# Performance work log

Measured on AMD Instinct MI355X. Metric: run time of the kernel, lower is better.

## Reference

```python
import jax, jax.numpy as jnp
import numpy as np

B, C, K, D = 2048, 100, 8, 64


def setup_inputs() -> dict:
    key = jax.random.key(0)
    k1, k2, k3, k4 = jax.random.split(key, 4)
    representation = jax.random.normal(k1, (B, D), dtype=jnp.float32)
    mixture_logits = 0.1 * jax.random.normal(k2, (C, K), dtype=jnp.float32)
    loc = jax.random.normal(k3, (C, K, D), dtype=jnp.float32)
    # lower-triangular with unit diagonal, small off-diagonal (matches 'random'/'zeros' init style)
    raw = 0.05 * jax.random.normal(k4, (C, K, D, D), dtype=jnp.float32)
    scale_tril = jnp.tril(raw, k=-1) + jnp.eye(D, dtype=jnp.float32)
    return {"representation": representation, "mixture_logits": mixture_logits,
            "loc": loc, "scale_tril": scale_tril}


def reference(representation, mixture_logits, loc, scale_tril):
    # representation: [B, D]; mixture_logits: [C, K]; loc: [C, K, D]; scale_tril: [C, K, D, D]
    d = representation.shape[-1]
    log2pi = jnp.log(jnp.asarray(2.0 * np.pi, dtype=representation.dtype))
    # residuals: [B, C, K, D] -> move batch last for batched triangular solve: [C, K, D, B]
    diff = representation[:, None, None, :] - loc[None]
    b = jnp.moveaxis(diff, 0, -1)
    # whiten: solve L z = (x - mu) for each (class, component)
    z = jax.lax.linalg.triangular_solve(scale_tril, b, left_side=True, lower=True)  # [C, K, D, B]
    quad = jnp.sum(z * z, axis=2)  # [C, K, B]
    # log|det Sigma|^{1/2} = sum log |diag(L)|
    logdet = jnp.sum(jnp.log(jnp.abs(jnp.diagonal(scale_tril, axis1=-2, axis2=-1))), axis=-1)  # [C, K]
    comp_lp = -0.5 * (quad + d * log2pi) - logdet[..., None]  # [C, K, B]
    mix = jax.nn.log_softmax(mixture_logits, axis=-1)  # [C, K]
    class_lp = jax.scipy.special.logsumexp(comp_lp + mix[..., None], axis=1)  # [C, B]
    logits = jax.nn.log_softmax(class_lp.T, axis=1)  # [B, C]
    return logits
```

## Files before the change

kernel.cpp:

```cpp
#include <hip/hip_runtime.h>
#include <math.h>

#define C_ 100
#define K_ 8
#define D_ 64
#define B_ 2048
#define BT_ 256

using f16x8 = __attribute__((ext_vector_type(8))) _Float16;
using f32x4 = __attribute__((ext_vector_type(4))) float;

#define LS_S 72
#define AT_S 65
__global__ __launch_bounds__(64, 1) void k_invert(const float* __restrict__ L_g,
                                                  const float* __restrict__ loc_g,
                                                  const float* __restrict__ ml,
                                                  f16x8* __restrict__ ATf,
                                                  float* __restrict__ v_g,
                                                  float* __restrict__ off_g) {
    const int ck = blockIdx.x;
    const int j = threadIdx.x;
    __shared__ float Ls[D_][LS_S];
    __shared__ float At[D_][AT_S];
    __shared__ float mus[D_];

    {
        const int c8 = (ck >> 3) << 3;
        const float mlj = ml[c8 + (j & 7)];
        float mx = mlj;
        mx = fmaxf(mx, __shfl_xor(mx, 1, 64));
        mx = fmaxf(mx, __shfl_xor(mx, 2, 64));
        mx = fmaxf(mx, __shfl_xor(mx, 4, 64));
        float se = __expf(mlj - mx);
        se += __shfl_xor(se, 1, 64);
        se += __shfl_xor(se, 2, 64);
        se += __shfl_xor(se, 4, 64);
        const float lse = mx + __logf(se);
        if (j == (ck & 7)) off_g[ck] = mlj - lse - 58.8120661251f;
    }

    const float4* Lsrc4 = reinterpret_cast<const float4*>(L_g + (size_t)ck * D_ * D_);
#pragma unroll
    for (int t = 0; t < 16; ++t) {
        const int idx = t * 64 + j;
        const float4 f = Lsrc4[idx];
        *reinterpret_cast<float4*>(&Ls[idx >> 4][(idx & 15) << 2]) = f;
    }
    mus[j] = loc_g[ck * D_ + j];
    __syncthreads();

    float a[D_];
#pragma unroll
    for (int m = 0; m < D_; ++m) a[m] = (j == m) ? 1.f : 0.f;

#pragma unroll
    for (int i = 1; i < D_; ++i) {
        float a0 = 0.f, a1 = 0.f, a2 = 0.f, a3 = 0.f;
#pragma unroll
        for (int m0 = 0; m0 + 3 < i; m0 += 4) {
            const float4 L4 = *reinterpret_cast<const float4*>(&Ls[i][m0]);
            a0 = fmaf(L4.x, a[m0 + 0], a0);
            a1 = fmaf(L4.y, a[m0 + 1], a1);
            a2 = fmaf(L4.z, a[m0 + 2], a2);
            a3 = fmaf(L4.w, a[m0 + 3], a3);
        }
#pragma unroll
        for (int m = i & ~3; m < i; ++m) a0 = fmaf(Ls[i][m], a[m], a0);
        const float nv = -((a0 + a1) + (a2 + a3));
        a[i] = (j < i) ? nv : a[i];
    }

#pragma unroll
    for (int m = 0; m < D_; ++m) At[m][j] = a[m];
    __syncthreads();

    const int q8 = (j >> 4) * 8, cl = j & 15;
    float vpart[4];
#pragma unroll
    for (int dt = 0; dt < 4; ++dt) {
        vpart[dt] = 0.f;
#pragma unroll
        for (int ks = 0; ks < 2; ++ks) {
            f16x8 t;
#pragma unroll
            for (int s = 0; s < 8; ++s) {
                const _Float16 h = (_Float16)At[dt * 16 + cl][ks * 32 + q8 + s];
                t[s] = h;
                vpart[dt] = fmaf((float)h, mus[ks * 32 + q8 + s], vpart[dt]);
            }
            ATf[(size_t)ck * 512 + (dt * 2 + ks) * 64 + j] = t;
        }
        vpart[dt] += __shfl_xor(vpart[dt], 16, 64);
        vpart[dt] += __shfl_xor(vpart[dt], 32, 64);
    }
    if (j < 16) {
#pragma unroll
        for (int dt = 0; dt < 4; ++dt)
            v_g[(size_t)ck * D_ + dt * 16 + j] = vpart[dt];
    }
}

__global__ __launch_bounds__(256, 3) void k_main(const float* __restrict__ rep,
                                                 const f16x8* __restrict__ ATf,
                                                 const float* __restrict__ v_g,
                                                 const float* __restrict__ off_g,
                                                 float* __restrict__ clp_g) {
    const int c = blockIdx.y;
    const int b0 = blockIdx.x * BT_;
    const int tid = threadIdx.x;
    const int w = tid >> 6;
    const int lane = tid & 63;
    const int col = lane & 15;
    const int quad = lane >> 4;

    __shared__ f16x8 Xs[BT_ * 8];
    __shared__ float qk[K_][BT_ + 4];
    __shared__ float offs_s[K_];

    if (tid < K_) offs_s[tid] = off_g[c * K_ + tid];

#pragma unroll
    for (int p = 0; p < BT_ / 32; ++p) {
        const int u = p * 256 + tid;
        const int q = u & 7, row = u >> 3;
        const float* xr = rep + (size_t)(b0 + row) * D_ + q * 8;
        const float4 x0 = *reinterpret_cast<const float4*>(xr);
        const float4 x1 = *reinterpret_cast<const float4*>(xr + 4);
        f16x8 val;
        val[0] = (_Float16)x0.x; val[1] = (_Float16)x0.y;
        val[2] = (_Float16)x0.z; val[3] = (_Float16)x0.w;
        val[4] = (_Float16)x1.x; val[5] = (_Float16)x1.y;
        val[6] = (_Float16)x1.z; val[7] = (_Float16)x1.w;
        const int s = row >> 5, bt = (row >> 4) & 1, cc = row & 15;
        Xs[((s * 2 + bt) * 8 + q) * 16 + (q ^ cc)] = val;
    }
    __syncthreads();

#pragma unroll 1
    for (int half = 0; half < 2; ++half) {
        const int k = w + half * 4;
        const int ck = c * K_ + k;
        f16x8 Af[8];
#pragma unroll
        for (int f = 0; f < 8; ++f)
            Af[f] = ATf[(size_t)ck * 512 + f * 64 + lane];
        f32x4 vvn[4];
#pragma unroll
        for (int dt = 0; dt < 4; ++dt)
            vvn[dt] = -(*reinterpret_cast<const f32x4*>(
                v_g + (size_t)ck * D_ + dt * 16 + quad * 4));

#pragma unroll 1
        for (int s = 0; s < BT_ / 32; ++s) {
            f16x8 Xf[2][2];
#pragma unroll
            for (int bt = 0; bt < 2; ++bt)
#pragma unroll
                for (int ks = 0; ks < 2; ++ks) {
                    const int q = ks * 4 + quad;
                    Xf[bt][ks] = Xs[((s * 2 + bt) * 8 + q) * 16 + (q ^ col)];
                }

            f32x4 acc[2][4];
#pragma unroll
            for (int bt = 0; bt < 2; ++bt)
#pragma unroll
                for (int dt = 0; dt < 4; ++dt) {
                    acc[bt][dt] = __builtin_amdgcn_mfma_f32_16x16x32_f16(
                        Af[dt * 2 + 0], Xf[bt][0], vvn[dt], 0, 0, 0);
                    acc[bt][dt] = __builtin_amdgcn_mfma_f32_16x16x32_f16(
                        Af[dt * 2 + 1], Xf[bt][1], acc[bt][dt], 0, 0, 0);
                }

#pragma unroll
            for (int bt = 0; bt < 2; ++bt) {
                float p = 0.f;
#pragma unroll
                for (int dt = 0; dt < 4; ++dt)
#pragma unroll
                    for (int r = 0; r < 4; ++r)
                        p = fmaf(acc[bt][dt][r], acc[bt][dt][r], p);
                p += __shfl_xor(p, 16, 64);
                p += __shfl_xor(p, 32, 64);
                if (quad == 0)
                    qk[k][s * 32 + bt * 16 + col] = p;
            }
        }
    }
    __syncthreads();

    {
        float lp[K_];
        float m = -INFINITY;
#pragma unroll
        for (int k = 0; k < K_; ++k) {
            lp[k] = fmaf(-0.5f, qk[k][tid], offs_s[k]);
            m = fmaxf(m, lp[k]);
        }
        float s = 0.f;
#pragma unroll
        for (int k = 0; k < K_; ++k) s += __expf(lp[k] - m);
        clp_g[(size_t)c * B_ + b0 + tid] = m + __logf(s);
    }
}

__global__ __launch_bounds__(256) void k_final(const float* __restrict__ clp,
                                               float* __restrict__ out) {
    const int wave = threadIdx.x >> 6;
    const int lane = threadIdx.x & 63;
    const int b = blockIdx.x * 4 + wave;
    const float x0 = clp[(size_t)lane * B_ + b];
    const float x1 = (lane < C_ - 64) ? clp[(size_t)(64 + lane) * B_ + b] : -INFINITY;
    float m = fmaxf(x0, x1);
    for (int o = 32; o > 0; o >>= 1) m = fmaxf(m, __shfl_xor(m, o, 64));
    float s = __expf(x0 - m) + ((lane < C_ - 64) ? __expf(x1 - m) : 0.f);
    for (int o = 32; o > 0; o >>= 1) s += __shfl_xor(s, o, 64);
    const float L = m + __logf(s);
    out[(size_t)b * C_ + lane] = x0 - L;
    if (lane < C_ - 64) out[(size_t)b * C_ + 64 + lane] = x1 - L;
}

extern "C" void kernel_launch(void* const* d_in, const int* in_sizes, int n_in,
                              void* d_out, int out_size, void* d_ws, size_t ws_size,
                              hipStream_t stream) {
    const float* rep = (const float*)d_in[0];
    const float* ml  = (const float*)d_in[1];
    const float* loc = (const float*)d_in[2];
    const float* st  = (const float*)d_in[3];
    float* out = (float*)d_out;

    char* w = (char*)d_ws;
    f16x8* ATf = (f16x8*)w;
    float* v   = (float*)(w + 6553600);
    float* off = (float*)(w + 6758400);
    float* clp = (float*)(w + 6761600);

    k_invert<<<dim3(C_ * K_), dim3(64), 0, stream>>>(st, loc, ml, ATf, v, off);
    k_main<<<dim3(B_ / BT_, C_), dim3(256), 0, stream>>>(rep, ATf, v, off, clp);
    k_final<<<dim3(B_ / 4), dim3(256), 0, stream>>>(clp, out);
}
```

Before: 104.9 us.

## Fuse final log-softmax into main kernel via last-block atomic counter

Removes the separate k_final launch. Each batch tile now keeps a completion counter that k_invert zeroes, and the last class block to finish a tile does the cross-class log-softmax and writes the output, reading through a transposed shared-memory tile. The batch tile is halved to 128 so there are twice as many blocks and occupancy can rise, and the first component's fragments are loaded before staging X. The cost is atomics, thread fences, and a serial tail of work on the last-arriving block of each tile.

```diff
diff --git a/kernel.cpp b/kernel.cpp
--- a/kernel.cpp
+++ b/kernel.cpp
@@ -5,7 +5,7 @@
 #define K_ 8
 #define D_ 64
 #define B_ 2048
-#define BT_ 256
+#define BT_ 128
 
 using f16x8 = __attribute__((ext_vector_type(8))) _Float16;
 using f32x4 = __attribute__((ext_vector_type(4))) float;
@@ -17,12 +17,15 @@
                                                   const float* __restrict__ ml,
                                                   f16x8* __restrict__ ATf,
                                                   float* __restrict__ v_g,
-                                                  float* __restrict__ off_g) {
+                                                  float* __restrict__ off_g,
+                                                  int* __restrict__ done_g) {
     const int ck = blockIdx.x;
     const int j = threadIdx.x;
     __shared__ float Ls[D_][LS_S];
     __shared__ float At[D_][AT_S];
     __shared__ float mus[D_];
+
+    if (j == 0 && ck < B_ / BT_) done_g[ck] = 0;
 
     {
         const int c8 = (ck >> 3) << 3;
@@ -100,11 +103,17 @@
     }
 }
 
-__global__ __launch_bounds__(256, 3) void k_main(const float* __restrict__ rep,
+#define SMA_QK 16384
+#define SMA_OFFS (SMA_QK + K_ * 132 * 4)
+#define SMB_L (64 * 105 * 4)
+#define SM_BYTES (SMB_L + 64 * 4)
+__global__ __launch_bounds__(256, 4) void k_main(const float* __restrict__ rep,
                                                  const f16x8* __restrict__ ATf,
                                                  const float* __restrict__ v_g,
                                                  const float* __restrict__ off_g,
-                                                 float* __restrict__ clp_g) {
+                                                 float* __restrict__ clp_g,
+                                                 int* __restrict__ done_g,
+                                                 float* __restrict__ out) {
     const int c = blockIdx.y;
     const int b0 = blockIdx.x * BT_;
     const int tid = threadIdx.x;
@@ -113,14 +122,29 @@
     const int col = lane & 15;
     const int quad = lane >> 4;
 
-    __shared__ f16x8 Xs[BT_ * 8];
-    __shared__ float qk[K_][BT_ + 4];
-    __shared__ float offs_s[K_];
+    __shared__ __align__(16) char smraw[SM_BYTES];
+    __shared__ int isLast;
+    f16x8* Xs = reinterpret_cast<f16x8*>(smraw);
+    float(*qk)[132] = reinterpret_cast<float(*)[132]>(smraw + SMA_QK);
+    float* offs_s = reinterpret_cast<float*>(smraw + SMA_OFFS);
+    float(*T)[105] = reinterpret_cast<float(*)[105]>(smraw);
+    float* Lrow = reinterpret_cast<float*>(smraw + SMB_L);
+
+    const int ck0 = c * K_ + w;
+    f16x8 Af[8];
+#pragma unroll
+    for (int f = 0; f < 8; ++f)
+        Af[f] = ATf[(size_t)ck0 * 512 + f * 64 + lane];
+    f32x4 vvn[4];
+#pragma unroll
+    for (int dt = 0; dt < 4; ++dt)
+        vvn[dt] = -(*reinterpret_cast<const f32x4*>(
+            v_g + (size_t)ck0 * D_ + dt * 16 + quad * 4));
 
     if (tid < K_) offs_s[tid] = off_g[c * K_ + tid];
 
 #pragma unroll
-    for (int p = 0; p < BT_ / 32; ++p) {
+    for (int p = 0; p < 4; ++p) {
         const int u = p * 256 + tid;
         const int q = u & 7, row = u >> 3;
         const float* xr = rep + (size_t)(b0 + row) * D_ + q * 8;
@@ -139,19 +163,19 @@
 #pragma unroll 1
     for (int half = 0; half < 2; ++half) {
         const int k = w + half * 4;
-        const int ck = c * K_ + k;
-        f16x8 Af[8];
-#pragma unroll
-        for (int f = 0; f < 8; ++f)
-            Af[f] = ATf[(size_t)ck * 512 + f * 64 + lane];
-        f32x4 vvn[4];
-#pragma unroll
-        for (int dt = 0; dt < 4; ++dt)
-            vvn[dt] = -(*reinterpret_cast<const f32x4*>(
-                v_g + (size_t)ck * D_ + dt * 16 + quad * 4));
-
-#pragma unroll 1
-        for (int s = 0; s < BT_ / 32; ++s) {
+        if (half == 1) {
+            const int ck = c * K_ + k;
+#pragma unroll
+            for (int f = 0; f < 8; ++f)
+                Af[f] = ATf[(size_t)ck * 512 + f * 64 + lane];
+#pragma unroll
+            for (int dt = 0; dt < 4; ++dt)
+                vvn[dt] = -(*reinterpret_cast<const f32x4*>(
+                    v_g + (size_t)ck * D_ + dt * 16 + quad * 4));
+        }
+
+#pragma unroll 1
+        for (int s = 0; s < 4; ++s) {
             f16x8 Xf[2][2];
 #pragma unroll
             for (int bt = 0; bt < 2; ++bt)
@@ -189,7 +213,7 @@
     }
     __syncthreads();
 
-    {
+    if (tid < BT_) {
         float lp[K_];
         float m = -INFINITY;
 #pragma unroll
@@ -202,22 +226,46 @@
         for (int k = 0; k < K_; ++k) s += __expf(lp[k] - m);
         clp_g[(size_t)c * B_ + b0 + tid] = m + __logf(s);
     }
-}
-
-__global__ __launch_bounds__(256) void k_final(const float* __restrict__ clp,
-                                               float* __restrict__ out) {
-    const int wave = threadIdx.x >> 6;
-    const int lane = threadIdx.x & 63;
-    const int b = blockIdx.x * 4 + wave;
-    const float x0 = clp[(size_t)lane * B_ + b];
-    const float x1 = (lane < C_ - 64) ? clp[(size_t)(64 + lane) * B_ + b] : -INFINITY;
-    float m = fmaxf(x0, x1);
-    for (int o = 32; o > 0; o >>= 1) m = fmaxf(m, __shfl_xor(m, o, 64));
-    float s = __expf(x0 - m) + ((lane < C_ - 64) ? __expf(x1 - m) : 0.f);
-    for (int o = 32; o > 0; o >>= 1) s += __shfl_xor(s, o, 64);
-    const float L = m + __logf(s);
-    out[(size_t)b * C_ + lane] = x0 - L;
-    if (lane < C_ - 64) out[(size_t)b * C_ + 64 + lane] = x1 - L;
+
+    __threadfence();
+    __syncthreads();
+    if (tid == 0) {
+        const int prev = atomicAdd(&done_g[blockIdx.x], 1);
+        isLast = (prev == C_ - 1);
+    }
+    __syncthreads();
+    if (!isLast) return;
+    __threadfence();
+
+#pragma unroll 1
+    for (int ch = 0; ch < 2; ++ch) {
+        const int bb = b0 + ch * 64;
+#pragma unroll 1
+        for (int cb = 0; cb < C_; cb += 4) {
+            const int cc = cb + (tid >> 6);
+            const int bl = tid & 63;
+            T[bl][cc] = clp_g[(size_t)cc * B_ + bb + bl];
+        }
+        __syncthreads();
+        if (tid < 64) {
+            float m = -INFINITY;
+#pragma unroll 4
+            for (int cc = 0; cc < C_; ++cc) m = fmaxf(m, T[tid][cc]);
+            float s = 0.f;
+#pragma unroll 4
+            for (int cc = 0; cc < C_; ++cc) s += __expf(T[tid][cc] - m);
+            Lrow[tid] = m + __logf(s);
+        }
+        __syncthreads();
+#pragma unroll 1
+        for (int r0 = 0; r0 < 64; r0 += 2) {
+            const int r = r0 + (tid >> 7);
+            const int cc = tid & 127;
+            if (cc < C_)
+                out[(size_t)(bb + r) * C_ + cc] = T[r][cc] - Lrow[r];
+        }
+        __syncthreads();
+    }
 }
 
 extern "C" void kernel_launch(void* const* d_in, const int* in_sizes, int n_in,
@@ -234,8 +282,8 @@
     float* v   = (float*)(w + 6553600);
     float* off = (float*)(w + 6758400);
     float* clp = (float*)(w + 6761600);
-
-    k_invert<<<dim3(C_ * K_), dim3(64), 0, stream>>>(st, loc, ml, ATf, v, off);
-    k_main<<<dim3(B_ / BT_, C_), dim3(256), 0, stream>>>(rep, ATf, v, off, clp);
-    k_final<<<dim3(B_ / 4), dim3(256), 0, stream>>>(clp, out);
+    int* done  = (int*)(w + 7580800);
+
+    k_invert<<<dim3(C_ * K_), dim3(64), 0, stream>>>(st, loc, ml, ATf, v, off, done);
+    k_main<<<dim3(B_ / BT_, C_), dim3(256), 0, stream>>>(rep, ATf, v, off, clp, done, out);
 }
```

Result: slower. 260.7 us (+148.7%).
